# Kernel tuning notes

Measured on AMD Instinct MI355X. Metric: run time of the kernel, lower is better.

## Reference

```python
import jax, jax.numpy as jnp
import numpy as np

HEAD_SIZE = 64
EPS_GN = 1e-5 * 8 * 8  # GroupNorm eps = 1e-5 * head_size_divisor**2


def rwkv7_scan(w_raw, q, k, v, a, b):
    """RWKV-7 'wind backstepping' linear recurrence.
    Inputs [B,T,H,N]. Per step (matching the CUDA kernel):
      decay = exp(-exp(w_raw)); sa = S @ a; S = S*decay + sa b^T + v k^T; y = S @ q
    State S is [B,H,N_value,N_key]."""
    decay = jnp.exp(-jnp.exp(w_raw))
    B, T, H, N = q.shape
    xs = tuple(jnp.moveaxis(t, 1, 0) for t in (decay, q, k, v, a, b))  # [T,B,H,N]
    S0 = jnp.zeros((B, H, N, N), q.dtype)

    def step(S, inp):
        d, qt, kt, vt, at, bt = inp
        sa = jnp.einsum('bhij,bhj->bhi', S, at)
        S = S * d[:, :, None, :] + sa[..., None] * bt[:, :, None, :] + vt[..., None] * kt[:, :, None, :]
        y = jnp.einsum('bhij,bhj->bhi', S, qt)
        return S, y

    _, ys = jax.lax.scan(step, S0, xs)
    return jnp.moveaxis(ys, 0, 1)  # [B,T,H,N]


def setup_inputs() -> dict:
    key = jax.random.key(0)
    B, T, C, H, N = 4, 960, 2048, 32, 64
    Dw, Da, Dv, Dg = 96, 96, 64, 256
    ks = iter(jax.random.split(key, 40))

    def nrm(shape, s=0.02):
        return jax.random.normal(next(ks), shape, jnp.float32) * s

    def uni(shape):
        return jax.random.uniform(next(ks), shape, jnp.float32)

    return dict(
        x=nrm((B, T, C), 1.0),
        v_first=nrm((B, T, C), 1.0),
        x_r=uni((1, 1, C)), x_w=uni((1, 1, C)), x_k=uni((1, 1, C)),
        x_v=uni((1, 1, C)), x_a=uni((1, 1, C)), x_g=uni((1, 1, C)),
        w0=jnp.linspace(-7.0, -2.0, C, dtype=jnp.float32).reshape(1, 1, C) + 0.5,
        w1=nrm((C, Dw)), w2=nrm((Dw, C)),
        a0=nrm((1, 1, C)), a1=nrm((C, Da)), a2=nrm((Da, C)),
        v0=jnp.ones((1, 1, C), jnp.float32), v1=nrm((C, Dv)), v2=nrm((Dv, C)),
        g1=nrm((C, Dg)), g2=nrm((Dg, C)),
        k_k=jnp.full((1, 1, C), 0.85, jnp.float32),
        k_a=jnp.ones((1, 1, C), jnp.float32),
        r_k=nrm((H, N)),
        Wr=nrm((C, C)), Wk=nrm((C, C)), Wv=nrm((C, C)), Wo=nrm((C, C)),
        ln_w=jnp.ones((C,), jnp.float32), ln_b=jnp.zeros((C,), jnp.float32),
    )


def reference(x, v_first, x_r, x_w, x_k, x_v, x_a, x_g,
              w0, w1, w2, a0, a1, a2, v0, v1, v2, g1, g2,
              k_k, k_a, r_k, Wr, Wk, Wv, Wo, ln_w, ln_b):
    B, T, C = x.shape
    H = C // HEAD_SIZE
    # time_shift: ZeroPad2d((0,0,1,-1)) == shift right by 1 along T with zero at t=0
    x_prev = jnp.pad(x, ((0, 0), (1, 0), (0, 0)))[:, :T]
    xx = x_prev - x
    xr = x + xx * x_r; xw = x + xx * x_w; xk = x + xx * x_k
    xv = x + xx * x_v; xa = x + xx * x_a; xg = x + xx * x_g

    r = xr @ Wr.T
    w = -jax.nn.softplus(-(w0 + jnp.tanh(xw @ w1) @ w2)) - 0.5
    k = xk @ Wk.T
    v = xv @ Wv.T
    # layer_id != 0: residual-value mixing with first layer's value
    v = v + (v_first - v) * jax.nn.sigmoid(v0 + (xv @ v1) @ v2)
    a = jax.nn.sigmoid(a0 + (xa @ a1) @ a2)
    g = jax.nn.sigmoid(xg @ g1) @ g2

    kk = (k * k_k).reshape(B, T, H, HEAD_SIZE)
    kk = kk / jnp.maximum(jnp.linalg.norm(kk, axis=-1, keepdims=True), 1e-12)  # F.normalize
    kk = kk.reshape(B, T, C)
    k = k * (1 + (a - 1) * k_a)

    hs = lambda t: t.reshape(B, T, H, HEAD_SIZE)
    y = rwkv7_scan(hs(w), hs(r), hs(k), hs(v), hs(-kk), hs(kk * a)).reshape(B, T, C)

    # GroupNorm(H groups over C)
    yg = y.reshape(B, T, H, HEAD_SIZE)
    mu = yg.mean(-1, keepdims=True)
    var = yg.var(-1, keepdims=True)
    y = ((yg - mu) / jnp.sqrt(var + EPS_GN)).reshape(B, T, C) * ln_w + ln_b

    y = y + ((hs(r) * hs(k) * r_k).sum(-1, keepdims=True) * hs(v)).reshape(B, T, C)
    return (y * g) @ Wo.T
```

## Files before the change

kernel.cpp:

```cpp
#include <hip/hip_runtime.h>
#include <stdint.h>

#define BDIM 4
#define TDIM 960
#define CDIM 2048
#define HDIM 32
#define NDIM 64
#define BT   (BDIM*TDIM)

typedef unsigned short u16;
typedef __attribute__((ext_vector_type(8))) short short8;
typedef __attribute__((ext_vector_type(4))) float f32x4;

__device__ __forceinline__ float b2f(u16 u){
  union{unsigned int i; float f;}x; x.i=((unsigned int)u)<<16; return x.f;
}
__device__ __forceinline__ u16 f2b(float f){
  union{float f; unsigned int i;}x; x.f=f;
  unsigned int r = x.i + 0x7fffu + ((x.i>>16)&1u);
  return (u16)(r>>16);
}
__device__ __forceinline__ void unpack8(uint4 p, float* o){
  o[0]=b2f((u16)(p.x&0xffff)); o[1]=b2f((u16)(p.x>>16));
  o[2]=b2f((u16)(p.y&0xffff)); o[3]=b2f((u16)(p.y>>16));
  o[4]=b2f((u16)(p.z&0xffff)); o[5]=b2f((u16)(p.z>>16));
  o[6]=b2f((u16)(p.w&0xffff)); o[7]=b2f((u16)(p.w>>16));
}
__device__ __forceinline__ uint4 pack8(const float* o){
  uint4 p;
  p.x = (unsigned)f2b(o[0]) | ((unsigned)f2b(o[1])<<16);
  p.y = (unsigned)f2b(o[2]) | ((unsigned)f2b(o[3])<<16);
  p.z = (unsigned)f2b(o[4]) | ((unsigned)f2b(o[5])<<16);
  p.w = (unsigned)f2b(o[6]) | ((unsigned)f2b(o[7])<<16);
  return p;
}
__device__ __forceinline__ void ld8f(const float* p, float* o){
  float4 a = *(const float4*)p;
  float4 b = *(const float4*)(p+4);
  o[0]=a.x;o[1]=a.y;o[2]=a.z;o[3]=a.w;o[4]=b.x;o[5]=b.y;o[6]=b.z;o[7]=b.w;
}
__device__ __forceinline__ float sigm(float x){ return 1.f/(1.f+expf(-x)); }
__device__ __forceinline__ void stc(float* p, float v){ *p = v; }
__device__ __forceinline__ void stc(u16* p, float v){ *p = f2b(v); }

__global__ __launch_bounds__(256) void cvt_kernel(const float* src, u16* dst){
  size_t i = ((size_t)blockIdx.x*256 + threadIdx.x)*8;
  float v[8]; ld8f(src+i, v);
  *(uint4*)(dst+i) = pack8(v);
}

struct TJob { const float* src; u16* dst; int R, Cs, DR, DC; };
struct TJobs8 { TJob j[8]; };

__global__ __launch_bounds__(256) void transpose_pad_kernel(TJobs8 jobs){
  TJob jb = jobs.j[blockIdx.z];
  int idx = blockIdx.x*256 + threadIdx.x;
  int total = jb.DR*jb.DC;
  if (idx >= total) return;
  int i = idx / jb.DC, k = idx % jb.DC;
  float v = 0.f;
  if (i < jb.Cs && k < jb.R) v = jb.src[(size_t)k*jb.Cs + i];
  jb.dst[idx] = f2b(v);
}

__global__ __launch_bounds__(256) void mix_kernel(
  const float* x,
  const float* cr, const float* cw, const float* ck,
  const float* cv, const float* ca, const float* cg,
  u16* mr, u16* mw, u16* mk, u16* mv, u16* ma, u16* mg)
{
  size_t tid = (size_t)blockIdx.x*256 + threadIdx.x;
  size_t base = tid*8;
  int c = (int)(base % CDIM);
  int row = (int)(base / CDIM);
  int t = row % TDIM;
  float xc[8], xp[8], xx[8], cf[8], o[8];
  ld8f(x+base, xc);
  if (t > 0) {
    ld8f(x+base-CDIM, xp);
  } else {
    for(int j=0;j<8;j++) xp[j]=0.f;
  }
  #pragma unroll
  for(int j=0;j<8;j++) xx[j]=xp[j]-xc[j];
#define DOMIX(CP, OP) do { ld8f(CP+c, cf); \
  _Pragma("unroll") for(int j=0;j<8;j++) o[j]=xc[j]+xx[j]*cf[j]; \
  *(uint4*)(OP+base)=pack8(o); } while(0)
  DOMIX(cr, mr); DOMIX(cw, mw); DOMIX(ck, mk);
  DOMIX(cv, mv); DOMIX(ca, ma); DOMIX(cg, mg);
#undef DOMIX
}

struct GemmJob {
  const u16* A; const u16* Bt; void* C;
  int nbm, nbn, K, lda, ldb, ldc;
};
struct GemmJobs { GemmJob j[4]; };

template<typename TC>
__global__ __launch_bounds__(256, 2) void gemm_bt_kernel(GemmJobs jobs){
  GemmJob jb = jobs.j[blockIdx.z];
  int bm = blockIdx.x % jb.nbm;
  int bn = blockIdx.x / jb.nbm;
  if (bn >= jb.nbn) return;
  __shared__ __attribute__((aligned(16))) u16 As[128*64];
  __shared__ __attribute__((aligned(16))) u16 Bs[128*64];
  int tid = threadIdx.x;
  int wave = tid>>6, lane = tid&63;
  int wr = wave>>1, wc = wave&1;
  f32x4 acc[4][4];
  #pragma unroll
  for(int i=0;i<4;i++)
    #pragma unroll
    for(int j=0;j<4;j++) acc[i][j] = (f32x4){0.f,0.f,0.f,0.f};
  const int rA0 = bm*128;
  const int rB0 = bn*128;
  int srow = (lane>>3);
  int scol = (lane&7)*8;
  for (int k0=0; k0<jb.K; k0+=64){
    #pragma unroll
    for (int it=0; it<4; ++it){
      int rr = wave*32 + it*8;
      const u16* gA = jb.A + (size_t)(rA0 + rr + srow)*jb.lda + (k0 + scol);
      __builtin_amdgcn_global_load_lds((const __attribute__((address_space(1))) void*)gA,
          (__attribute__((address_space(3))) void*)&As[rr*64], 16, 0, 0);
      const u16* gB = jb.Bt + (size_t)(rB0 + rr + srow)*jb.ldb + (k0 + scol);
      __builtin_amdgcn_global_load_lds((const __attribute__((address_space(1))) void*)gB,
          (__attribute__((address_space(3))) void*)&Bs[rr*64], 16, 0, 0);
    }
    __syncthreads();
    #pragma unroll
    for (int kc=0; kc<2; ++kc){
      short8 af[4], bfr[4];
      int ko = kc*32 + (lane>>4)*8;
      #pragma unroll
      for (int mi=0; mi<4; ++mi)
        af[mi] = *(const short8*)&As[(wr*64 + mi*16 + (lane&15))*64 + ko];
      #pragma unroll
      for (int ni=0; ni<4; ++ni)
        bfr[ni] = *(const short8*)&Bs[(wc*64 + ni*16 + (lane&15))*64 + ko];
      #pragma unroll
      for (int mi=0; mi<4; ++mi)
        #pragma unroll
        for (int ni=0; ni<4; ++ni)
          acc[mi][ni] = __builtin_amdgcn_mfma_f32_16x16x32_bf16(af[mi], bfr[ni], acc[mi][ni], 0, 0, 0);
    }
    __syncthreads();
  }
  TC* C = (TC*)jb.C;
  int cn = (lane&15);
  int rq = (lane>>4)*4;
  #pragma unroll
  for (int mi=0; mi<4; ++mi){
    #pragma unroll
    for (int ni=0; ni<4; ++ni){
      int col = rB0 + wc*64 + ni*16 + cn;
      int row = rA0 + wr*64 + mi*16 + rq;
      #pragma unroll
      for (int e=0; e<4; ++e)
        stc(&C[(size_t)(row+e)*jb.ldc + col], acc[mi][ni][e]);
    }
  }
}

__global__ __launch_bounds__(256) void act_kernel(u16* hw, u16* hg){
  int idx = blockIdx.x*256 + threadIdx.x;
  if (blockIdx.z==0){ if (idx < BT*128) hw[idx] = f2b(tanhf(b2f(hw[idx]))); }
  else              { if (idx < BT*256) hg[idx] = f2b(sigm(b2f(hg[idx]))); }
}

__global__ __launch_bounds__(256) void post_kernel(
  const u16* kbuf, const u16* vraw, const float* vfirst,
  const u16* wl, const u16* al, const u16* vl,
  const float* w0, const float* a0, const float* v0,
  const float* kkc, const float* kac,
  float* dout, u16* ks, u16* vs, u16* as_, u16* bs)
{
  int row = blockIdx.x, tid = threadIdx.x;
  int c = tid*8;
  size_t base = (size_t)row*CDIM + c;
  float kf[8], vr[8], vf[8], wlf[8], alf[8], vlf[8], w0f[8], a0f[8], v0f[8], kkf[8], kaf[8];
  unpack8(*(const uint4*)(kbuf+base), kf);
  unpack8(*(const uint4*)(vraw+base), vr);
  ld8f(vfirst+base, vf);
  unpack8(*(const uint4*)(wl+base), wlf);
  unpack8(*(const uint4*)(al+base), alf);
  unpack8(*(const uint4*)(vl+base), vlf);
  ld8f(w0+c, w0f);
  ld8f(a0+c, a0f);
  ld8f(v0+c, v0f);
  ld8f(kkc+c, kkf);
  ld8f(kac+c, kaf);
  float dv[8], av[8], vv[8], kkr[8], kfin[8], asv[8], bsv[8];
  float ssq = 0.f;
  #pragma unroll
  for (int j=0;j<8;j++){
    float wv = -log1pf(expf(-(w0f[j]+wlf[j]))) - 0.5f;
    dv[j]  = expf(-expf(wv));
    av[j]  = sigm(a0f[j]+alf[j]);
    vv[j]  = vr[j] + (vf[j]-vr[j])*sigm(v0f[j]+vlf[j]);
    kkr[j] = kf[j]*kkf[j];
    ssq   += kkr[j]*kkr[j];
    kfin[j]= kf[j]*(1.f + (av[j]-1.f)*kaf[j]);
  }
  ssq += __shfl_xor(ssq,1); ssq += __shfl_xor(ssq,2); ssq += __shfl_xor(ssq,4);
  float inv = 1.f/fmaxf(sqrtf(ssq), 1e-12f);
  #pragma unroll
  for (int j=0;j<8;j++){ float kkn = kkr[j]*inv; asv[j] = -kkn; bsv[j] = kkn*av[j]; }
  *(float4*)(dout+base)   = make_float4(dv[0],dv[1],dv[2],dv[3]);
  *(float4*)(dout+base+4) = make_float4(dv[4],dv[5],dv[6],dv[7]);
  *(uint4*)(ks+base)  = pack8(kfin);
  *(uint4*)(vs+base)  = pack8(vv);
  *(uint4*)(as_+base) = pack8(asv);
  *(uint4*)(bs+base)  = pack8(bsv);
}

__global__ __launch_bounds__(256, 2) void scan_kernel(
  const float* decayp, const u16* qb, const u16* kb, const u16* vb,
  const u16* ab, const u16* bb, float* yb)
{
  const int DEC=0, QQ=512, KK=1024, AA=1536, BB=2048, VV=2560, BUF=2688;
  __shared__ float sb[2*2688];
  int blk = blockIdx.x;
  int b    = blk >> 7;
  int h    = (blk >> 2) & 31;
  int qtr  = blk & 3;
  int tid = threadIdx.x;
  int jg = tid & 15;
  int ii = tid >> 4;
  int row0 = qtr*16;
  int row = row0 + ii;
  int lst = tid >> 5;
  int lc  = tid & 31;
  size_t hbase = ((size_t)b*TDIM)*CDIM + (size_t)h*NDIM;

  float S[4];
  #pragma unroll
  for (int e=0;e<4;e++) S[e]=0.f;

  float2 dreg; unsigned qreg, kreg, areg, breg; u16 vreg=0;
  auto load_group = [&](int t0){
    size_t g = hbase + (size_t)(t0+lst)*CDIM + lc*2;
    dreg = *(const float2*)(decayp + g);
    qreg = *(const unsigned*)(qb + g);
    kreg = *(const unsigned*)(kb + g);
    areg = *(const unsigned*)(ab + g);
    breg = *(const unsigned*)(bb + g);
    if (lc < 16) vreg = vb[hbase + (size_t)(t0+lst)*CDIM + row0 + lc];
  };
  auto store_group = [&](int p){
    float* buf = &sb[p*BUF];
    *(float2*)&buf[DEC + lst*64 + lc*2] = dreg;
    *(float2*)&buf[QQ  + lst*64 + lc*2] = make_float2(b2f((u16)(qreg&0xffff)), b2f((u16)(qreg>>16)));
    *(float2*)&buf[KK  + lst*64 + lc*2] = make_float2(b2f((u16)(kreg&0xffff)), b2f((u16)(kreg>>16)));
    *(float2*)&buf[AA  + lst*64 + lc*2] = make_float2(b2f((u16)(areg&0xffff)), b2f((u16)(areg>>16)));
    *(float2*)&buf[BB  + lst*64 + lc*2] = make_float2(b2f((u16)(breg&0xffff)), b2f((u16)(breg>>16)));
    if (lc < 16) buf[VV + lst*16 + lc] = b2f(vreg);
  };

  load_group(0);
  store_group(0);
  __syncthreads();
  int p = 0;
  for (int g=0; g<120; ++g){
    if (g+1 < 120) load_group((g+1)*8);
    const float* buf = &sb[p*BUF];
    float yp[8];
    #pragma unroll
    for (int s=0; s<8; ++s){
      f32x4 a0 = *(const f32x4*)&buf[AA + s*64 + jg*4];
      float sap = (S[0]*a0[0] + S[1]*a0[1]) + (S[2]*a0[2] + S[3]*a0[3]);
      sap += __shfl_xor(sap,1);
      sap += __shfl_xor(sap,2);
      sap += __shfl_xor(sap,4);
      sap += __shfl_xor(sap,8);
      f32x4 d0 = *(const f32x4*)&buf[DEC + s*64 + jg*4];
      f32x4 k0 = *(const f32x4*)&buf[KK  + s*64 + jg*4];
      f32x4 b0 = *(const f32x4*)&buf[BB  + s*64 + jg*4];
      f32x4 q0 = *(const f32x4*)&buf[QQ  + s*64 + jg*4];
      float vi = buf[VV + s*16 + ii];
      #pragma unroll
      for (int e=0;e<4;e++)
        S[e] = S[e]*d0[e] + sap*b0[e] + vi*k0[e];
      yp[s] = (S[0]*q0[0] + S[1]*q0[1]) + (S[2]*q0[2] + S[3]*q0[3]);
    }
    #pragma unroll
    for (int s=0; s<8; ++s){
      yp[s] += __shfl_xor(yp[s],1);
      yp[s] += __shfl_xor(yp[s],2);
      yp[s] += __shfl_xor(yp[s],4);
      yp[s] += __shfl_xor(yp[s],8);
    }
    if (jg < 8){
      float out = 0.f;
      #pragma unroll
      for (int s=0; s<8; ++s) if (jg==s) out = yp[s];
      yb[hbase + (size_t)(g*8+jg)*CDIM + row] = out;
    }
    if (g+1 < 120) store_group(p^1);
    __syncthreads();
    p ^= 1;
  }
}

__global__ __launch_bounds__(256) void final_kernel(
  const float* yb, const u16* rb, const u16* ks, const u16* vs,
  const float* rk, const float* lnw, const float* lnb, const u16* gl, u16* yg)
{
  int row = blockIdx.x, tid = threadIdx.x;
  int c = tid*8;
  size_t base = (size_t)row*CDIM + c;
  float y[8], rf[8], kf[8], vf[8], rkf[8], lw[8], lb[8], gf[8];
  ld8f(yb+base, y);
  unpack8(*(const uint4*)(rb+base), rf);
  unpack8(*(const uint4*)(ks+base), kf);
  unpack8(*(const uint4*)(vs+base), vf);
  ld8f(rk+c,  rkf);
  ld8f(lnw+c, lw);
  ld8f(lnb+c, lb);
  unpack8(*(const uint4*)(gl+base), gf);
  float sy=0.f, syy=0.f, coef=0.f;
  #pragma unroll
  for (int j=0;j<8;j++){ sy+=y[j]; syy+=y[j]*y[j]; coef += rf[j]*kf[j]*rkf[j]; }
  sy  += __shfl_xor(sy,1);  sy  += __shfl_xor(sy,2);  sy  += __shfl_xor(sy,4);
  syy += __shfl_xor(syy,1); syy += __shfl_xor(syy,2); syy += __shfl_xor(syy,4);
  coef+= __shfl_xor(coef,1);coef+= __shfl_xor(coef,2);coef+= __shfl_xor(coef,4);
  float mu  = sy*(1.f/64.f);
  float var = syy*(1.f/64.f) - mu*mu;
  float rs  = rsqrtf(var + 6.4e-4f);
  float o[8];
  #pragma unroll
  for (int j=0;j<8;j++)
    o[j] = (((y[j]-mu)*rs)*lw[j] + lb[j] + coef*vf[j]) * gf[j];
  *(uint4*)(yg+base) = pack8(o);
}

extern "C" void kernel_launch(void* const* d_in, const int* in_sizes, int n_in,
                              void* d_out, int out_size, void* d_ws, size_t ws_size,
                              hipStream_t stream)
{
  const float* x      = (const float*)d_in[0];
  const float* vfirst = (const float*)d_in[1];
  const float* c_r = (const float*)d_in[2];
  const float* c_w = (const float*)d_in[3];
  const float* c_k = (const float*)d_in[4];
  const float* c_v = (const float*)d_in[5];
  const float* c_a = (const float*)d_in[6];
  const float* c_g = (const float*)d_in[7];
  const float* w0i = (const float*)d_in[8];
  const float* w1i = (const float*)d_in[9];
  const float* w2i = (const float*)d_in[10];
  const float* a0i = (const float*)d_in[11];
  const float* a1i = (const float*)d_in[12];
  const float* a2i = (const float*)d_in[13];
  const float* v0i = (const float*)d_in[14];
  const float* v1i = (const float*)d_in[15];
  const float* v2i = (const float*)d_in[16];
  const float* g1i = (const float*)d_in[17];
  const float* g2i = (const float*)d_in[18];
  const float* kki = (const float*)d_in[19];
  const float* kai = (const float*)d_in[20];
  const float* rki = (const float*)d_in[21];
  const float* Wr  = (const float*)d_in[22];
  const float* Wk  = (const float*)d_in[23];
  const float* Wv  = (const float*)d_in[24];
  const float* Wo  = (const float*)d_in[25];
  const float* lnw = (const float*)d_in[26];
  const float* lnb = (const float*)d_in[27];

  char* ws = (char*)d_ws;
  const size_t S2 = (size_t)BT*CDIM*2;
  u16* MIXR = (u16*)(ws + 0*S2);
  u16* MIXW = (u16*)(ws + 1*S2);
  u16* MIXK = (u16*)(ws + 2*S2);
  u16* MIXV = (u16*)(ws + 3*S2);
  u16* MIXA = (u16*)(ws + 4*S2);
  u16* MIXG = (u16*)(ws + 5*S2);
  u16* RBUF = (u16*)(ws + 6*S2);
  u16* KBUF = (u16*)(ws + 7*S2);
  u16* VRAW = (u16*)(ws + 8*S2);
  char* WB = ws + 9*S2;
  u16* WSLOT = (u16*)WB;
  char* WT = WB + 8388608;
  u16* W1T = (u16*)(WT + 0);
  u16* A1T = (u16*)(WT + 524288);
  u16* V1T = (u16*)(WT + 1048576);
  u16* G1T = (u16*)(WT + 1572864);
  u16* W2T = (u16*)(WT + 2621440);
  u16* A2T = (u16*)(WT + 3145728);
  u16* V2T = (u16*)(WT + 3670016);
  u16* G2T = (u16*)(WT + 4194304);
  char* HB = WT + 5242880;
  u16* HW = (u16*)(HB + 0);
  u16* HA = (u16*)(HB + 983040);
  u16* HV = (u16*)(HB + 1966080);
  u16* HG = (u16*)(HB + 2949120);
  char* L2 = HB + 4915200;
  u16* WL = (u16*)(L2 + 0*S2);
  u16* AL = (u16*)(L2 + 1*S2);
  u16* VL = (u16*)(L2 + 2*S2);
  u16* GL = (u16*)(L2 + 3*S2);
  float* WDEC = (float*)(ws + 0*S2);
  u16* KS = (u16*)(ws + 2*S2);
  u16* VS = (u16*)(ws + 3*S2);
  u16* AS = (u16*)(ws + 4*S2);
  u16* BS = (u16*)(ws + 5*S2);
  float* YBUF = (float*)(L2 + 0*S2);
  u16* YG = (u16*)(L2 + 2*S2);
  (void)in_sizes; (void)n_in; (void)out_size; (void)ws_size;

  TJobs8 tj;
  tj.j[0] = (TJob){w1i, W1T, 2048,  96, 128, 2048};
  tj.j[1] = (TJob){a1i, A1T, 2048,  96, 128, 2048};
  tj.j[2] = (TJob){v1i, V1T, 2048,  64, 128, 2048};
  tj.j[3] = (TJob){g1i, G1T, 2048, 256, 256, 2048};
  tj.j[4] = (TJob){w2i, W2T,   96, 2048, 2048, 128};
  tj.j[5] = (TJob){a2i, A2T,   96, 2048, 2048, 128};
  tj.j[6] = (TJob){v2i, V2T,   64, 2048, 2048, 128};
  tj.j[7] = (TJob){g2i, G2T,  256, 2048, 2048, 256};
  transpose_pad_kernel<<<dim3(2048,1,8), 256, 0, stream>>>(tj);

  mix_kernel<<<dim3(BT*CDIM/8/256), 256, 0, stream>>>(
      x, c_r, c_w, c_k, c_v, c_a, c_g, MIXR, MIXW, MIXK, MIXV, MIXA, MIXG);

  {
    GemmJobs gj;
    cvt_kernel<<<dim3(2048), 256, 0, stream>>>(Wr, WSLOT);
    gj.j[0] = (GemmJob){MIXR, WSLOT, RBUF, 30, 16, 2048, 2048, 2048, 2048};
    gj.j[1] = gj.j[0]; gj.j[2] = gj.j[0]; gj.j[3] = gj.j[0];
    gemm_bt_kernel<u16><<<dim3(480,1,1), 256, 0, stream>>>(gj);
    cvt_kernel<<<dim3(2048), 256, 0, stream>>>(Wk, WSLOT);
    gj.j[0] = (GemmJob){MIXK, WSLOT, KBUF, 30, 16, 2048, 2048, 2048, 2048};
    gemm_bt_kernel<u16><<<dim3(480,1,1), 256, 0, stream>>>(gj);
    cvt_kernel<<<dim3(2048), 256, 0, stream>>>(Wv, WSLOT);
    gj.j[0] = (GemmJob){MIXV, WSLOT, VRAW, 30, 16, 2048, 2048, 2048, 2048};
    gemm_bt_kernel<u16><<<dim3(480,1,1), 256, 0, stream>>>(gj);
  }

  GemmJobs lj1;
  lj1.j[0] = (GemmJob){MIXW, W1T, HW, 30, 1, 2048, 2048, 2048, 128};
  lj1.j[1] = (GemmJob){MIXA, A1T, HA, 30, 1, 2048, 2048, 2048, 128};
  lj1.j[2] = (GemmJob){MIXV, V1T, HV, 30, 1, 2048, 2048, 2048, 128};
  lj1.j[3] = (GemmJob){MIXG, G1T, HG, 30, 2, 2048, 2048, 2048, 256};
  gemm_bt_kernel<u16><<<dim3(60,1,4), 256, 0, stream>>>(lj1);

  act_kernel<<<dim3(3840,1,2), 256, 0, stream>>>(HW, HG);

  GemmJobs lj2;
  lj2.j[0] = (GemmJob){HW, W2T, WL, 30, 16, 128, 128, 128, 2048};
  lj2.j[1] = (GemmJob){HA, A2T, AL, 30, 16, 128, 128, 128, 2048};
  lj2.j[2] = (GemmJob){HV, V2T, VL, 30, 16, 128, 128, 128, 2048};
  lj2.j[3] = (GemmJob){HG, G2T, GL, 30, 16, 256, 256, 256, 2048};
  gemm_bt_kernel<u16><<<dim3(480,1,4), 256, 0, stream>>>(lj2);

  post_kernel<<<dim3(BT), 256, 0, stream>>>(
      KBUF, VRAW, vfirst, WL, AL, VL, w0i, a0i, v0i, kki, kai,
      WDEC, KS, VS, AS, BS);

  scan_kernel<<<dim3(512), 256, 0, stream>>>(
      WDEC, RBUF, KS, VS, AS, BS, YBUF);

  final_kernel<<<dim3(BT), 256, 0, stream>>>(
      YBUF, RBUF, KS, VS, rki, lnw, lnb, GL, YG);

  cvt_kernel<<<dim3(2048), 256, 0, stream>>>(Wo, WSLOT);
  GemmJobs oj;
  oj.j[0] = (GemmJob){YG, WSLOT, d_out, 30, 16, 2048, 2048, 2048, 2048};
  oj.j[1] = oj.j[0]; oj.j[2] = oj.j[0]; oj.j[3] = oj.j[0];
  gemm_bt_kernel<float><<<dim3(480,1,1), 256, 0, stream>>>(oj);
}
```

Measured before the change: 889.1 us.

## Replace LDS double-buffered scan staging with register prefetch and DPP reductions

```diff
diff --git a/kernel.cpp b/kernel.cpp
--- a/kernel.cpp
+++ b/kernel.cpp
@@ -42,6 +42,14 @@
 __device__ __forceinline__ float sigm(float x){ return 1.f/(1.f+expf(-x)); }
 __device__ __forceinline__ void stc(float* p, float v){ *p = v; }
 __device__ __forceinline__ void stc(u16* p, float v){ *p = f2b(v); }
+
+__device__ __forceinline__ float row_red16(float x){
+  x += __int_as_float(__builtin_amdgcn_update_dpp(0, __float_as_int(x), 0xB1,  0xF, 0xF, true));
+  x += __int_as_float(__builtin_amdgcn_update_dpp(0, __float_as_int(x), 0x4E,  0xF, 0xF, true));
+  x += __int_as_float(__builtin_amdgcn_update_dpp(0, __float_as_int(x), 0x141, 0xF, 0xF, true));
+  x += __int_as_float(__builtin_amdgcn_update_dpp(0, __float_as_int(x), 0x140, 0xF, 0xF, true));
+  return x;
+}
 
 __global__ __launch_bounds__(256) void cvt_kernel(const float* src, u16* dst){
   size_t i = ((size_t)blockIdx.x*256 + threadIdx.x)*8;
@@ -216,11 +224,11 @@
 }
 
 __global__ __launch_bounds__(256, 2) void scan_kernel(
-  const float* decayp, const u16* qb, const u16* kb, const u16* vb,
-  const u16* ab, const u16* bb, float* yb)
+  const float* __restrict__ decayp, const u16* __restrict__ qb,
+  const u16* __restrict__ kb, const u16* __restrict__ vb,
+  const u16* __restrict__ ab, const u16* __restrict__ bb,
+  float* __restrict__ yb)
 {
-  const int DEC=0, QQ=512, KK=1024, AA=1536, BB=2048, VV=2560, BUF=2688;
-  __shared__ float sb[2*2688];
   int blk = blockIdx.x;
   int b    = blk >> 7;
   int h    = (blk >> 2) & 31;
@@ -228,78 +236,60 @@
   int tid = threadIdx.x;
   int jg = tid & 15;
   int ii = tid >> 4;
-  int row0 = qtr*16;
-  int row = row0 + ii;
-  int lst = tid >> 5;
-  int lc  = tid & 31;
+  int row = qtr*16 + ii;
   size_t hbase = ((size_t)b*TDIM)*CDIM + (size_t)h*NDIM;
 
-  float S[4];
-  #pragma unroll
-  for (int e=0;e<4;e++) S[e]=0.f;
-
-  float2 dreg; unsigned qreg, kreg, areg, breg; u16 vreg=0;
-  auto load_group = [&](int t0){
-    size_t g = hbase + (size_t)(t0+lst)*CDIM + lc*2;
-    dreg = *(const float2*)(decayp + g);
-    qreg = *(const unsigned*)(qb + g);
-    kreg = *(const unsigned*)(kb + g);
-    areg = *(const unsigned*)(ab + g);
-    breg = *(const unsigned*)(bb + g);
-    if (lc < 16) vreg = vb[hbase + (size_t)(t0+lst)*CDIM + row0 + lc];
+  const float* dp = decayp + hbase + jg*4;
+  const u16*  qp = qb + hbase + jg*4;
+  const u16*  kp = kb + hbase + jg*4;
+  const u16*  ap = ab + hbase + jg*4;
+  const u16*  bp = bb + hbase + jg*4;
+  const u16*  vp = vb + hbase + row;
+
+  float S[4] = {0.f, 0.f, 0.f, 0.f};
+
+  struct StepRegs { f32x4 d; ushort4 q, k, a, b; u16 v; };
+  auto loadstep = [&](int t)->StepRegs{
+    StepRegs r;
+    size_t off = (size_t)t*CDIM;
+    r.d = *(const f32x4*)(dp + off);
+    r.q = *(const ushort4*)(qp + off);
+    r.k = *(const ushort4*)(kp + off);
+    r.a = *(const ushort4*)(ap + off);
+    r.b = *(const ushort4*)(bp + off);
+    r.v = vp[off];
+    return r;
   };
-  auto store_group = [&](int p){
-    float* buf = &sb[p*BUF];
-    *(float2*)&buf[DEC + lst*64 + lc*2] = dreg;
-    *(float2*)&buf[QQ  + lst*64 + lc*2] = make_float2(b2f((u16)(qreg&0xffff)), b2f((u16)(qreg>>16)));
-    *(float2*)&buf[KK  + lst*64 + lc*2] = make_float2(b2f((u16)(kreg&0xffff)), b2f((u16)(kreg>>16)));
-    *(float2*)&buf[AA  + lst*64 + lc*2] = make_float2(b2f((u16)(areg&0xffff)), b2f((u16)(areg>>16)));
-    *(float2*)&buf[BB  + lst*64 + lc*2] = make_float2(b2f((u16)(breg&0xffff)), b2f((u16)(breg>>16)));
-    if (lc < 16) buf[VV + lst*16 + lc] = b2f(vreg);
+  auto dostep = [&](const StepRegs& r)->float{
+    float a0=b2f(r.a.x), a1=b2f(r.a.y), a2=b2f(r.a.z), a3=b2f(r.a.w);
+    float sap = (S[0]*a0 + S[1]*a1) + (S[2]*a2 + S[3]*a3);
+    sap = row_red16(sap);
+    float k0=b2f(r.k.x), k1=b2f(r.k.y), k2=b2f(r.k.z), k3=b2f(r.k.w);
+    float c0=b2f(r.b.x), c1=b2f(r.b.y), c2=b2f(r.b.z), c3=b2f(r.b.w);
+    float vi=b2f(r.v);
+    S[0] = S[0]*r.d[0] + sap*c0 + vi*k0;
+    S[1] = S[1]*r.d[1] + sap*c1 + vi*k1;
+    S[2] = S[2]*r.d[2] + sap*c2 + vi*k2;
+    S[3] = S[3]*r.d[3] + sap*c3 + vi*k3;
+    return (S[0]*b2f(r.q.x) + S[1]*b2f(r.q.y)) + (S[2]*b2f(r.q.z) + S[3]*b2f(r.q.w));
   };
 
-  load_group(0);
-  store_group(0);
-  __syncthreads();
-  int p = 0;
+  StepRegs R0 = loadstep(0), R1 = loadstep(1), R2 = loadstep(2), R3 = loadstep(3);
   for (int g=0; g<120; ++g){
-    if (g+1 < 120) load_group((g+1)*8);
-    const float* buf = &sb[p*BUF];
     float yp[8];
+#define STEP(RR, S_) { int t_ = g*8 + (S_); int tn_ = t_+4 < TDIM ? t_+4 : TDIM-1; \
+    StepRegs nn_ = loadstep(tn_); yp[S_] = dostep(RR); RR = nn_; }
+    STEP(R0,0) STEP(R1,1) STEP(R2,2) STEP(R3,3)
+    STEP(R0,4) STEP(R1,5) STEP(R2,6) STEP(R3,7)
+#undef STEP
     #pragma unroll
-    for (int s=0; s<8; ++s){
-      f32x4 a0 = *(const f32x4*)&buf[AA + s*64 + jg*4];
-      float sap = (S[0]*a0[0] + S[1]*a0[1]) + (S[2]*a0[2] + S[3]*a0[3]);
-      sap += __shfl_xor(sap,1);
-      sap += __shfl_xor(sap,2);
-      sap += __shfl_xor(sap,4);
-      sap += __shfl_xor(sap,8);
-      f32x4 d0 = *(const f32x4*)&buf[DEC + s*64 + jg*4];
-      f32x4 k0 = *(const f32x4*)&buf[KK  + s*64 + jg*4];
-      f32x4 b0 = *(const f32x4*)&buf[BB  + s*64 + jg*4];
-      f32x4 q0 = *(const f32x4*)&buf[QQ  + s*64 + jg*4];
-      float vi = buf[VV + s*16 + ii];
-      #pragma unroll
-      for (int e=0;e<4;e++)
-        S[e] = S[e]*d0[e] + sap*b0[e] + vi*k0[e];
-      yp[s] = (S[0]*q0[0] + S[1]*q0[1]) + (S[2]*q0[2] + S[3]*q0[3]);
-    }
-    #pragma unroll
-    for (int s=0; s<8; ++s){
-      yp[s] += __shfl_xor(yp[s],1);
-      yp[s] += __shfl_xor(yp[s],2);
-      yp[s] += __shfl_xor(yp[s],4);
-      yp[s] += __shfl_xor(yp[s],8);
-    }
+    for (int s=0; s<8; ++s) yp[s] = row_red16(yp[s]);
     if (jg < 8){
       float out = 0.f;
       #pragma unroll
       for (int s=0; s<8; ++s) if (jg==s) out = yp[s];
       yb[hbase + (size_t)(g*8+jg)*CDIM + row] = out;
     }
-    if (g+1 < 120) store_group(p^1);
-    __syncthreads();
-    p ^= 1;
   }
 }
 
```

Result: no change. 897.7 us (+1.0%).
